# Optimization experiments

Measured on AMD Instinct MI355X. Metric: run time of the kernel, lower is better.

Reference implementation:

```python
import jax, jax.numpy as jnp
import numpy as np

B, L, A = 16, 32, 2046
M = A + 2  # user col + attributors + item col = 2048 nodes


def _xavier_uniform(key, shape, gain):
    fan_out, fan_in = shape  # torch 2D param: fan_in = shape[1], fan_out = shape[0]
    bound = gain * np.sqrt(6.0 / (fan_in + fan_out))
    return jax.random.uniform(key, shape, jnp.float32, -bound, bound)


def setup_inputs() -> dict:
    key = jax.random.key(0)
    k = jax.random.split(key, 7)
    user = jax.random.normal(k[0], (B, 6 * L, 1), jnp.float32)
    item = jax.random.normal(k[1], (B, 6 * L, 1), jnp.float32)
    attributor = jax.random.normal(k[2], (B, 6 * L, A), jnp.float32)
    adj = (jax.random.uniform(k[3], (M, M)) < 0.5).astype(jnp.float32)
    initial_weight = jax.random.normal(k[4], (M, M), jnp.float32)
    W_1 = _xavier_uniform(k[5], (6 * L, A), gain=np.sqrt(2.0))  # relu gain
    W_2 = _xavier_uniform(k[6], (6 * L, L), gain=1.44)
    return {"user": user, "item": item, "attributor": attributor,
            "adj": adj, "initial_weight": initial_weight,
            "W_1": W_1, "W_2": W_2}


def reference(user, item, attributor, adj, initial_weight, W_1, W_2):
    N = W_2.shape[1]  # = length L
    a = attributor * W_1                                   # (B, 6L, A)
    raw = jnp.concatenate([user, a, item], axis=2)         # (B, 6L, M)
    Q, K, V = jnp.split(raw, 3, axis=1)                    # each (B, 2L, M)
    r = jax.nn.relu
    # (relu(X).T @ W).T  ==  einsum over the 2L dim -> (B, L, M)
    Query = jnp.einsum('bnm,nl->blm', r(Q), W_2[:2 * N])
    Key = jnp.einsum('bnm,nl->blm', r(K), W_2[2 * N:4 * N])
    Value = jnp.einsum('bnm,nl->blm', r(V), W_2[4 * N:])
    # h = Query.mT @ Key * adj * initial_weight  -> (B, M, M)
    h = jnp.einsum('blm,bln->bmn', Query, Key) * adj * initial_weight
    d = h - jnp.swapaxes(h, -1, -2)
    exp_h = jnp.exp(jnp.where(d > 0, 0.0, d))              # exp(min(d, 0))
    causal = exp_h / (exp_h + jnp.swapaxes(exp_h, -1, -2)) * adj  # (B, M, M)
    Ans = Value @ causal                                    # (B, L, M)
    idx = jnp.array([0, Ans.shape[2] - 1])
    return Ans[:, :, idx]                                   # (B, L, 2)
```

## Files before the change

### kernel.cpp

```cpp
#include <hip/hip_runtime.h>
#include <math.h>

#define BB 16
#define LL 32
#define AA 2046
#define MM 2048
#define NROWS 192
#define CT 32
#define CPB 64


__global__ __launch_bounds__(256) void fused_kernel(
    const float* __restrict__ user, const float* __restrict__ item,
    const float* __restrict__ att, const float* __restrict__ adj,
    const float* __restrict__ iw, const float* __restrict__ W1,
    const float* __restrict__ W2, float* __restrict__ out) {
  const int ctile = blockIdx.x, b = blockIdx.y, tid = threadIdx.x;
  __shared__ float KQ[4][LL];
  __shared__ float uvs[4][64];
  __shared__ float stS[16][16][4][2];
  __shared__ float cs[2][CPB];
  __shared__ float gred[16][4][2];

  if (tid < 128) {
    const int q = tid >> 5, l = tid & 31;
    const float* __restrict__ src = (q == 0 || q == 2) ? user : item;
    const int rbase = (q < 2) ? 64 : 0;
    float acc = 0.f;
#pragma unroll
    for (int r = 0; r < 64; ++r)
      acc += fmaxf(src[b * NROWS + rbase + r], 0.f) * W2[(rbase + r) * LL + l];
    KQ[q][l] = acc;
  }
  __syncthreads();
  {
    const int which = tid >> 6, r = tid & 63;
    const int wrow = (which < 2) ? r : 64 + r;
    float acc = 0.f;
#pragma unroll
    for (int l = 0; l < LL; ++l) acc += W2[wrow * LL + l] * KQ[which][l];
    uvs[which][r] = acc;
  }
  __syncthreads();

  {
    const int cq = tid & 15, rg = tid >> 4;
    const int c0 = ctile * CPB + cq * 4;
    const float* __restrict__ wj0 = uvs[(rg < 8) ? 0 : 2];
    const float* __restrict__ wj1 = uvs[(rg < 8) ? 1 : 3];
    const int rbase = (rg < 8) ? 0 : 64;
    const int rrow0 = (rg & 7) * 8 + rbase;
    float a[4][2] = {};
#pragma unroll
    for (int i = 0; i < 8; ++i) {
      const int r = rrow0 + i;
      const int widx = r - rbase;
      const size_t arow = (size_t)(b * NROWS + r) * AA;
      const size_t wrow = (size_t)r * AA;
      const float2 av0 = *(const float2*)(att + arow + c0);
      const float2 wv0 = *(const float2*)(W1 + wrow + c0);
      const float v0 = fmaxf(av0.x * wv0.x, 0.f);
      const float v1 = fmaxf(av0.y * wv0.y, 0.f);
      float v2, v3;
      if (c0 + 2 < AA) {
        const float2 av1 = *(const float2*)(att + arow + c0 + 2);
        const float2 wv1 = *(const float2*)(W1 + wrow + c0 + 2);
        v2 = fmaxf(av1.x * wv1.x, 0.f);
        v3 = fmaxf(av1.y * wv1.y, 0.f);
      } else {
        v2 = fmaxf(user[b * NROWS + r], 0.f);
        v3 = fmaxf(item[b * NROWS + r], 0.f);
      }
      const float u0 = wj0[widx], u1 = wj1[widx];
      a[0][0] += v0 * u0; a[0][1] += v0 * u1;
      a[1][0] += v1 * u0; a[1][1] += v1 * u1;
      a[2][0] += v2 * u0; a[2][1] += v2 * u1;
      a[3][0] += v3 * u0; a[3][1] += v3 * u1;
    }
#pragma unroll
    for (int k = 0; k < 4; ++k) {
      stS[rg][cq][k][0] = a[k][0];
      stS[rg][cq][k][1] = a[k][1];
    }
  }
  __syncthreads();

  if (tid < 128) {
    const int col = tid >> 1, j = tid & 1;
    const int cq = col >> 2, ci = col & 3;
    float s = 0.f, t = 0.f;
#pragma unroll
    for (int rg = 0; rg < 8; ++rg) s += stS[rg][cq][ci][j];
#pragma unroll
    for (int rg = 8; rg < 16; ++rg) t += stS[rg][cq][ci][j];
    const int cc = ctile * CPB + col;
    const int n = (cc < AA) ? cc + 1 : ((cc == AA) ? 0 : MM - 1);
    const size_t tcol = j ? (MM - 1) : 0;
    const float an = adj[(size_t)n * MM + tcol];
    const float wn = an * iw[(size_t)n * MM + tcol];
    const float wt = adj[tcol * MM + n] * iw[tcol * MM + n];
    const float d = s * wn - t * wt;
    const float e = expf(-fabsf(d));
    const float sig = (d > 0.f) ? 1.f / (1.f + e) : e / (1.f + e);
    cs[j][col] = sig * an;
  }
  __syncthreads();

  {
    const int cq = tid & 15, rg = tid >> 4;
    const int c0 = ctile * CPB + cq * 4;
    const float c00 = cs[0][cq * 4], c01 = cs[0][cq * 4 + 1];
    const float c02 = cs[0][cq * 4 + 2], c03 = cs[0][cq * 4 + 3];
    const float c10 = cs[1][cq * 4], c11 = cs[1][cq * 4 + 1];
    const float c12 = cs[1][cq * 4 + 2], c13 = cs[1][cq * 4 + 3];
    float g[4][2] = {};
#pragma unroll
    for (int i = 0; i < 4; ++i) {
      const int r = 128 + rg * 4 + i;
      const size_t arow = (size_t)(b * NROWS + r) * AA;
      const size_t wrow = (size_t)r * AA;
      const float2 av0 = *(const float2*)(att + arow + c0);
      const float2 wv0 = *(const float2*)(W1 + wrow + c0);
      const float v0 = fmaxf(av0.x * wv0.x, 0.f);
      const float v1 = fmaxf(av0.y * wv0.y, 0.f);
      float v2, v3;
      if (c0 + 2 < AA) {
        const float2 av1 = *(const float2*)(att + arow + c0 + 2);
        const float2 wv1 = *(const float2*)(W1 + wrow + c0 + 2);
        v2 = fmaxf(av1.x * wv1.x, 0.f);
        v3 = fmaxf(av1.y * wv1.y, 0.f);
      } else {
        v2 = fmaxf(user[b * NROWS + r], 0.f);
        v3 = fmaxf(item[b * NROWS + r], 0.f);
      }
      g[i][0] += v0 * c00 + v1 * c01 + v2 * c02 + v3 * c03;
      g[i][1] += v0 * c10 + v1 * c11 + v2 * c12 + v3 * c13;
    }
#pragma unroll
    for (int m = 8; m >= 1; m >>= 1) {
#pragma unroll
      for (int i = 0; i < 4; ++i) {
        g[i][0] += __shfl_xor(g[i][0], m, 16);
        g[i][1] += __shfl_xor(g[i][1], m, 16);
      }
    }
    if (cq == 0) {
#pragma unroll
      for (int i = 0; i < 4; ++i) {
        gred[rg][i][0] = g[i][0];
        gred[rg][i][1] = g[i][1];
      }
    }
  }
  __syncthreads();

  if (tid < 64) {
    const int l = tid & 31, j = tid >> 5;
    float acc = 0.f;
#pragma unroll
    for (int rv = 0; rv < 64; ++rv)
      acc += W2[(128 + rv) * LL + l] * gred[rv >> 2][rv & 3][j];
    atomicAdd(&out[b * (LL * 2) + l * 2 + j], acc);
  }
}

extern "C" void kernel_launch(void* const* d_in, const int* in_sizes, int n_in,
                              void* d_out, int out_size, void* d_ws,
                              size_t ws_size, hipStream_t stream) {
  const float* user = (const float*)d_in[0];
  const float* item = (const float*)d_in[1];
  const float* att = (const float*)d_in[2];
  const float* adj = (const float*)d_in[3];
  const float* iw = (const float*)d_in[4];
  const float* W1 = (const float*)d_in[5];
  const float* W2 = (const float*)d_in[6];
  float* out = (float*)d_out;

  hipMemsetAsync(d_out, 0, sizeof(float) * (size_t)out_size, stream);
  fused_kernel<<<dim3(CT, BB), 256, 0, stream>>>(user, item, att, adj, iw, W1,
                                                 W2, out);
}
```

Baseline: 108.5 us.

## Halve column tile, double blocks, and hoist all global loads before reductions

Column tile per block drops from 64 to 32, which doubles the grid to 64x16 blocks, and each thread now covers fewer rows. All attributor/W1 loads, including the value rows used after the sigmoid stage, are issued up front into registers so their latency overlaps the earlier shared-memory reductions and barriers. This is meant to raise memory-level parallelism and occupancy on a bandwidth-bound kernel. In exchange it uses more registers per thread and does more redundant per-block prologue work (the KQ/uvs computation) and more atomics.

```diff
diff --git a/kernel.cpp b/kernel.cpp
--- a/kernel.cpp
+++ b/kernel.cpp
@@ -6,8 +6,8 @@
 #define AA 2046
 #define MM 2048
 #define NROWS 192
-#define CT 32
-#define CPB 64
+#define CT 64
+#define CPB 32
 
 
 __global__ __launch_bounds__(256) void fused_kernel(
@@ -18,9 +18,9 @@
   const int ctile = blockIdx.x, b = blockIdx.y, tid = threadIdx.x;
   __shared__ float KQ[4][LL];
   __shared__ float uvs[4][64];
-  __shared__ float stS[16][16][4][2];
+  __shared__ float stS[32][8][4][2];
   __shared__ float cs[2][CPB];
-  __shared__ float gred[16][4][2];
+  __shared__ float gred[32][2][2];
 
   if (tid < 128) {
     const int q = tid >> 5, l = tid & 31;
@@ -43,39 +43,66 @@
   }
   __syncthreads();
 
+  const int cq = tid & 7, rg = tid >> 3;
+  const int c0 = ctile * CPB + cq * 4;
+  const bool tail = (c0 + 2 >= AA);
+
+  float vst[4][4];
+  float vva[2][4];
+  const int sbase = (rg < 16) ? 0 : 64;
+  const int r0 = sbase + (rg & 15) * 4;
+#pragma unroll
+  for (int i = 0; i < 4; ++i) {
+    const int r = r0 + i;
+    const size_t arow = (size_t)(b * NROWS + r) * AA;
+    const size_t wrow = (size_t)r * AA;
+    const float2 av0 = *(const float2*)(att + arow + c0);
+    const float2 wv0 = *(const float2*)(W1 + wrow + c0);
+    vst[i][0] = fmaxf(av0.x * wv0.x, 0.f);
+    vst[i][1] = fmaxf(av0.y * wv0.y, 0.f);
+    if (!tail) {
+      const float2 av1 = *(const float2*)(att + arow + c0 + 2);
+      const float2 wv1 = *(const float2*)(W1 + wrow + c0 + 2);
+      vst[i][2] = fmaxf(av1.x * wv1.x, 0.f);
+      vst[i][3] = fmaxf(av1.y * wv1.y, 0.f);
+    } else {
+      vst[i][2] = fmaxf(user[b * NROWS + r], 0.f);
+      vst[i][3] = fmaxf(item[b * NROWS + r], 0.f);
+    }
+  }
+#pragma unroll
+  for (int i = 0; i < 2; ++i) {
+    const int r = 128 + rg * 2 + i;
+    const size_t arow = (size_t)(b * NROWS + r) * AA;
+    const size_t wrow = (size_t)r * AA;
+    const float2 av0 = *(const float2*)(att + arow + c0);
+    const float2 wv0 = *(const float2*)(W1 + wrow + c0);
+    vva[i][0] = fmaxf(av0.x * wv0.x, 0.f);
+    vva[i][1] = fmaxf(av0.y * wv0.y, 0.f);
+    if (!tail) {
+      const float2 av1 = *(const float2*)(att + arow + c0 + 2);
+      const float2 wv1 = *(const float2*)(W1 + wrow + c0 + 2);
+      vva[i][2] = fmaxf(av1.x * wv1.x, 0.f);
+      vva[i][3] = fmaxf(av1.y * wv1.y, 0.f);
+    } else {
+      vva[i][2] = fmaxf(user[b * NROWS + r], 0.f);
+      vva[i][3] = fmaxf(item[b * NROWS + r], 0.f);
+    }
+  }
+
   {
-    const int cq = tid & 15, rg = tid >> 4;
-    const int c0 = ctile * CPB + cq * 4;
-    const float* __restrict__ wj0 = uvs[(rg < 8) ? 0 : 2];
-    const float* __restrict__ wj1 = uvs[(rg < 8) ? 1 : 3];
-    const int rbase = (rg < 8) ? 0 : 64;
-    const int rrow0 = (rg & 7) * 8 + rbase;
+    const float* __restrict__ wj0 = uvs[(rg < 16) ? 0 : 2];
+    const float* __restrict__ wj1 = uvs[(rg < 16) ? 1 : 3];
     float a[4][2] = {};
 #pragma unroll
-    for (int i = 0; i < 8; ++i) {
-      const int r = rrow0 + i;
-      const int widx = r - rbase;
-      const size_t arow = (size_t)(b * NROWS + r) * AA;
-      const size_t wrow = (size_t)r * AA;
-      const float2 av0 = *(const float2*)(att + arow + c0);
-      const float2 wv0 = *(const float2*)(W1 + wrow + c0);
-      const float v0 = fmaxf(av0.x * wv0.x, 0.f);
-      const float v1 = fmaxf(av0.y * wv0.y, 0.f);
-      float v2, v3;
-      if (c0 + 2 < AA) {
-        const float2 av1 = *(const float2*)(att + arow + c0 + 2);
-        const float2 wv1 = *(const float2*)(W1 + wrow + c0 + 2);
-        v2 = fmaxf(av1.x * wv1.x, 0.f);
-        v3 = fmaxf(av1.y * wv1.y, 0.f);
-      } else {
-        v2 = fmaxf(user[b * NROWS + r], 0.f);
-        v3 = fmaxf(item[b * NROWS + r], 0.f);
+    for (int i = 0; i < 4; ++i) {
+      const int widx = (rg & 15) * 4 + i;
+      const float u0 = wj0[widx], u1 = wj1[widx];
+#pragma unroll
+      for (int k = 0; k < 4; ++k) {
+        a[k][0] += vst[i][k] * u0;
+        a[k][1] += vst[i][k] * u1;
       }
-      const float u0 = wj0[widx], u1 = wj1[widx];
-      a[0][0] += v0 * u0; a[0][1] += v0 * u1;
-      a[1][0] += v1 * u0; a[1][1] += v1 * u1;
-      a[2][0] += v2 * u0; a[2][1] += v2 * u1;
-      a[3][0] += v3 * u0; a[3][1] += v3 * u1;
     }
 #pragma unroll
     for (int k = 0; k < 4; ++k) {
@@ -85,14 +112,14 @@
   }
   __syncthreads();
 
-  if (tid < 128) {
+  if (tid < 64) {
     const int col = tid >> 1, j = tid & 1;
-    const int cq = col >> 2, ci = col & 3;
+    const int q = col >> 2, ci = col & 3;
     float s = 0.f, t = 0.f;
 #pragma unroll
-    for (int rg = 0; rg < 8; ++rg) s += stS[rg][cq][ci][j];
+    for (int g = 0; g < 16; ++g) s += stS[g][q][ci][j];
 #pragma unroll
-    for (int rg = 8; rg < 16; ++rg) t += stS[rg][cq][ci][j];
+    for (int g = 16; g < 32; ++g) t += stS[g][q][ci][j];
     const int cc = ctile * CPB + col;
     const int n = (cc < AA) ? cc + 1 : ((cc == AA) ? 0 : MM - 1);
     const size_t tcol = j ? (MM - 1) : 0;
@@ -107,46 +134,25 @@
   __syncthreads();
 
   {
-    const int cq = tid & 15, rg = tid >> 4;
-    const int c0 = ctile * CPB + cq * 4;
-    const float c00 = cs[0][cq * 4], c01 = cs[0][cq * 4 + 1];
-    const float c02 = cs[0][cq * 4 + 2], c03 = cs[0][cq * 4 + 3];
-    const float c10 = cs[1][cq * 4], c11 = cs[1][cq * 4 + 1];
-    const float c12 = cs[1][cq * 4 + 2], c13 = cs[1][cq * 4 + 3];
-    float g[4][2] = {};
+    float g[2][2];
 #pragma unroll
-    for (int i = 0; i < 4; ++i) {
-      const int r = 128 + rg * 4 + i;
-      const size_t arow = (size_t)(b * NROWS + r) * AA;
-      const size_t wrow = (size_t)r * AA;
-      const float2 av0 = *(const float2*)(att + arow + c0);
-      const float2 wv0 = *(const float2*)(W1 + wrow + c0);
-      const float v0 = fmaxf(av0.x * wv0.x, 0.f);
-      const float v1 = fmaxf(av0.y * wv0.y, 0.f);
-      float v2, v3;
-      if (c0 + 2 < AA) {
-        const float2 av1 = *(const float2*)(att + arow + c0 + 2);
-        const float2 wv1 = *(const float2*)(W1 + wrow + c0 + 2);
-        v2 = fmaxf(av1.x * wv1.x, 0.f);
-        v3 = fmaxf(av1.y * wv1.y, 0.f);
-      } else {
-        v2 = fmaxf(user[b * NROWS + r], 0.f);
-        v3 = fmaxf(item[b * NROWS + r], 0.f);
-      }
-      g[i][0] += v0 * c00 + v1 * c01 + v2 * c02 + v3 * c03;
-      g[i][1] += v0 * c10 + v1 * c11 + v2 * c12 + v3 * c13;
+    for (int i = 0; i < 2; ++i) {
+      g[i][0] = vva[i][0] * cs[0][cq * 4] + vva[i][1] * cs[0][cq * 4 + 1] +
+                vva[i][2] * cs[0][cq * 4 + 2] + vva[i][3] * cs[0][cq * 4 + 3];
+      g[i][1] = vva[i][0] * cs[1][cq * 4] + vva[i][1] * cs[1][cq * 4 + 1] +
+                vva[i][2] * cs[1][cq * 4 + 2] + vva[i][3] * cs[1][cq * 4 + 3];
     }
 #pragma unroll
-    for (int m = 8; m >= 1; m >>= 1) {
+    for (int m = 4; m >= 1; m >>= 1) {
 #pragma unroll
-      for (int i = 0; i < 4; ++i) {
-        g[i][0] += __shfl_xor(g[i][0], m, 16);
-        g[i][1] += __shfl_xor(g[i][1], m, 16);
+      for (int i = 0; i < 2; ++i) {
+        g[i][0] += __shfl_xor(g[i][0], m, 8);
+        g[i][1] += __shfl_xor(g[i][1], m, 8);
       }
     }
     if (cq == 0) {
 #pragma unroll
-      for (int i = 0; i < 4; ++i) {
+      for (int i = 0; i < 2; ++i) {
         gred[rg][i][0] = g[i][0];
         gred[rg][i][1] = g[i][1];
       }
@@ -159,7 +165,7 @@
     float acc = 0.f;
 #pragma unroll
     for (int rv = 0; rv < 64; ++rv)
-      acc += W2[(128 + rv) * LL + l] * gred[rv >> 2][rv & 3][j];
+      acc += W2[(128 + rv) * LL + l] * gred[rv >> 1][rv & 1][j];
     atomicAdd(&out[b * (LL * 2) + l * 2 + j], acc);
   }
 }
```

Measured after the change: 111.9 us. 3.1% more time.
